# Performance work log

Measured on AMD Instinct MI355X. Metric: run time of the kernel, lower is better.

Reference implementation:

```python
import jax, jax.numpy as jnp
import numpy as np

D_HEAD = 64
IGNORE = -100000.0


def setup_inputs() -> dict:
    key = jax.random.key(0)
    ks = jax.random.split(key, 5)
    B, S, D, H, M = 2, 2048, 768, 12, D_HEAD
    scale = 0.05  # 'random_normal' keras init stddev
    return {
        "x": jax.random.normal(ks[0], (B, S, D), jnp.float32),
        "W_Q": jax.random.normal(ks[1], (H, D, M), jnp.float32) * scale,
        "b_Q": jnp.zeros((H, M), jnp.float32),
        "W_K": jax.random.normal(ks[2], (H, D, M), jnp.float32) * scale,
        "b_K": jnp.zeros((H, M), jnp.float32),
        "W_V": jax.random.normal(ks[3], (H, D, M), jnp.float32) * scale,
        "b_V": jnp.zeros((H, M), jnp.float32),
        "W_O": jax.random.normal(ks[4], (H, M, D), jnp.float32) * scale,
        "b_O": jnp.zeros((D,), jnp.float32),
    }


def reference(x, W_Q, b_Q, W_K, b_K, W_V, b_V, W_O, b_O):
    # q,k,v: [b, s, h, m]
    q = jnp.einsum("bqd,hdm->bqhm", x, W_Q) + b_Q
    k = jnp.einsum("bkd,hdm->bkhm", x, W_K) + b_K
    v = jnp.einsum("bkd,hdm->bkhm", x, W_V) + b_V
    # scores: [b, h, q, k], scaled by 1/sqrt(d_head)
    scores = jnp.einsum("bqhm,bkhm->bhqk", q, k) / jnp.sqrt(
        jnp.asarray(D_HEAD, q.dtype)
    )
    S = x.shape[1]
    # causal mask: strictly-upper-triangular positions set to IGNORE (-1e5),
    # matching tf.where(mask == 1, IGNORE, scores)
    causal = jnp.arange(S)[:, None] >= jnp.arange(S)[None, :]  # [q, k]
    scores = jnp.where(causal[None, None, :, :], scores, jnp.asarray(IGNORE, scores.dtype))
    pattern = jax.nn.softmax(scores, axis=-1)
    z = jnp.einsum("bhqk,bkhm->bqhm", pattern, v)
    attn_out = jnp.einsum("bqhm,hmd->bqd", z, W_O) + b_O
    return attn_out
```

## Files before the change

### kernel.cpp

```cpp
#include <hip/hip_runtime.h>
#include <hip/hip_bf16.h>
#include <cstdint>
#include <cstddef>

#define B_ 2
#define S_ 2048
#define D_ 768
#define H_ 12
#define M_ 64
#define BS_ (B_ * S_)
#define NQKV_ 2304
#define NCHUNK_ 80
#define TOTCHUNK_ (24 * NCHUNK_)

typedef __attribute__((ext_vector_type(8))) short bf16x8;
typedef __attribute__((ext_vector_type(4))) float f32x4;

__device__ __forceinline__ unsigned short f2bu(float f) {
    __hip_bfloat16 h = __float2bfloat16(f);
    unsigned short u;
    __builtin_memcpy(&u, &h, 2);
    return u;
}
__device__ __forceinline__ unsigned pack2(float a, float b) {
    return (unsigned)f2bu(a) | ((unsigned)f2bu(b) << 16);
}

__device__ __forceinline__ bf16x8 ld16(const unsigned short* p) {
    p = (const unsigned short*)__builtin_assume_aligned(p, 16);
    bf16x8 v; __builtin_memcpy(&v, p, 16); return v;
}
__device__ __forceinline__ uint4 ld16u(const unsigned short* p) {
    p = (const unsigned short*)__builtin_assume_aligned(p, 16);
    uint4 v; __builtin_memcpy(&v, p, 16); return v;
}
__device__ __forceinline__ void st16(unsigned short* p, uint4 v) {
    p = (unsigned short*)__builtin_assume_aligned(p, 16);
    __builtin_memcpy(p, &v, 16);
}
__device__ __forceinline__ void st8(unsigned short* p, uint2 v) {
    p = (unsigned short*)__builtin_assume_aligned(p, 8);
    __builtin_memcpy(p, &v, 8);
}
__device__ __forceinline__ float4 ldf4(const float* p) {
    p = (const float*)__builtin_assume_aligned(p, 16);
    float4 v; __builtin_memcpy(&v, p, 16); return v;
}
__device__ __forceinline__ void async16(const unsigned short* g, unsigned short* l) {
    __builtin_amdgcn_global_load_lds(
        (const __attribute__((address_space(1))) void*)g,
        (__attribute__((address_space(3))) void*)l, 16, 0, 0);
}
__device__ __forceinline__ void b82f(uint4 u, float* o) {
    o[0] = __uint_as_float(u.x << 16); o[1] = __uint_as_float(u.x & 0xffff0000u);
    o[2] = __uint_as_float(u.y << 16); o[3] = __uint_as_float(u.y & 0xffff0000u);
    o[4] = __uint_as_float(u.z << 16); o[5] = __uint_as_float(u.z & 0xffff0000u);
    o[6] = __uint_as_float(u.w << 16); o[7] = __uint_as_float(u.w & 0xffff0000u);
}

#define NEG_BIG (-3.0e38f)

__global__ void prep(const float* __restrict__ WQ, const float* __restrict__ WK,
                     const float* __restrict__ WV, const float* __restrict__ WO,
                     const float* __restrict__ x,
                     unsigned short* __restrict__ WT,
                     unsigned short* __restrict__ WOT,
                     unsigned short* __restrict__ xb)
{
    const int bx = blockIdx.x;
    if (bx < 216) {
        const int xx = bx % 9, yy = bx / 9;
        const int c  = xx * 256 + threadIdx.x;
        const int k0 = yy * 32;
        const int which = c / D_;
        const int r = c - which * D_;
        const int h = r >> 6, m = r & 63;
        const float* Wsel = (which == 0) ? WQ : (which == 1) ? WK : WV;
        const float* src = Wsel + (size_t)h * D_ * M_ + m;
        unsigned short* dst = WT + (size_t)c * D_ + k0;
        for (int i = 0; i < 32; i += 8) {
            float wv[8];
#pragma unroll
            for (int j = 0; j < 8; j++) wv[j] = src[(size_t)(k0 + i + j) * M_];
            uint4 pu;
            pu.x = pack2(wv[0], wv[1]); pu.y = pack2(wv[2], wv[3]);
            pu.z = pack2(wv[4], wv[5]); pu.w = pack2(wv[6], wv[7]);
            st16(dst + i, pu);
        }
    } else if (bx < 288) {
        const int b2 = bx - 216;
        const int xx = b2 % 3, yy = b2 / 3;
        const int c  = xx * 256 + threadIdx.x;
        const int k0 = yy * 32;
        unsigned short* dst = WOT + (size_t)c * D_ + k0;
        for (int i = 0; i < 32; i += 8) {
            float wv[8];
#pragma unroll
            for (int j = 0; j < 8; j++) wv[j] = WO[(size_t)(k0 + i + j) * D_ + c];
            uint4 pu;
            pu.x = pack2(wv[0], wv[1]); pu.y = pack2(wv[2], wv[3]);
            pu.z = pack2(wv[4], wv[5]); pu.w = pack2(wv[6], wv[7]);
            st16(dst + i, pu);
        }
    } else {
        const size_t i = ((size_t)(bx - 288) * 256 + threadIdx.x) * 16;
#pragma unroll
        for (int p = 0; p < 2; p++) {
            float4 a0 = ldf4(x + i + p * 8), a1 = ldf4(x + i + p * 8 + 4);
            uint4 u;
            u.x = pack2(a0.x, a0.y); u.y = pack2(a0.z, a0.w);
            u.z = pack2(a1.x, a1.y); u.w = pack2(a1.z, a1.w);
            st16(xb + i + p * 8, u);
        }
    }
}

__global__ __launch_bounds__(256, 2) void qkv_gemm(
    const unsigned short* __restrict__ xb,
    const unsigned short* __restrict__ WT,
    const float* __restrict__ bQ, const float* __restrict__ bK,
    const float* __restrict__ bV,
    unsigned short* __restrict__ qo, unsigned short* __restrict__ ko,
    unsigned short* __restrict__ vt)
{
    const int row0 = blockIdx.x * 128;
    const int col0 = blockIdx.y * 128;
    const int t = threadIdx.x;
    const int w = t >> 6, lane = t & 63, quad = lane >> 4, l16 = lane & 15;
    const int wrow0 = (w & 1) * 64, wcol0 = (w >> 1) * 64;

    __shared__ unsigned short Alds[128 * 64];
    __shared__ unsigned short Blds[128 * 64];

    f32x4 acc[4][4] = {};

    const unsigned short* asrc[4];
    const unsigned short* bsrc[4];
    int ldsoff[4];
#pragma unroll
    for (int q = 0; q < 4; q++) {
        const int cq = w * 256 + q * 64 + lane;
        const int row = cq >> 3, c = cq & 7;
        const int cs = c ^ (row & 7);
        asrc[q] = xb + (size_t)(row0 + row) * D_ + cs * 8;
        bsrc[q] = WT + (size_t)(col0 + row) * D_ + cs * 8;
        ldsoff[q] = (w * 256 + q * 64) * 8;
    }
    const int swz = (l16 & 7);

    for (int k0 = 0; k0 < D_; k0 += 64) {
#pragma unroll
        for (int q = 0; q < 4; q++) async16(asrc[q] + k0, Alds + ldsoff[q]);
#pragma unroll
        for (int q = 0; q < 4; q++) async16(bsrc[q] + k0, Blds + ldsoff[q]);
        __syncthreads();

        bf16x8 af[4][2], bfm[4][2];
#pragma unroll
        for (int rt = 0; rt < 4; rt++) {
            const int row = wrow0 + rt * 16 + l16;
#pragma unroll
            for (int hh = 0; hh < 2; hh++)
                af[rt][hh] = ld16(&Alds[row * 64 + ((hh * 4 + quad) ^ swz) * 8]);
        }
#pragma unroll
        for (int st = 0; st < 4; st++) {
            const int row = wcol0 + st * 16 + l16;
#pragma unroll
            for (int hh = 0; hh < 2; hh++)
                bfm[st][hh] = ld16(&Blds[row * 64 + ((hh * 4 + quad) ^ swz) * 8]);
        }
#pragma unroll
        for (int rt = 0; rt < 4; rt++)
#pragma unroll
            for (int st = 0; st < 4; st++) {
                acc[rt][st] = __builtin_amdgcn_mfma_f32_16x16x32_bf16(
                    af[rt][0], bfm[st][0], acc[rt][st], 0, 0, 0);
                acc[rt][st] = __builtin_amdgcn_mfma_f32_16x16x32_bf16(
                    af[rt][1], bfm[st][1], acc[rt][st], 0, 0, 0);
            }
        __syncthreads();
    }

    const int which = col0 / D_;
    const int colin = col0 - which * D_;

    if (which < 2) {
        const float* bias = (which == 0) ? bQ : bK;
        unsigned short* outp = (which == 0) ? qo : ko;
        const float scale = (which == 0) ? 0.125f : 1.0f;
#pragma unroll
        for (int st = 0; st < 4; st++) {
            const int cl = colin + wcol0 + st * 16 + l16;
            const int h = cl >> 6, m = cl & 63;
            const float bval = bias[cl];
#pragma unroll
            for (int rt = 0; rt < 4; rt++)
#pragma unroll
                for (int rr = 0; rr < 4; rr++) {
                    const int R = row0 + wrow0 + rt * 16 + quad * 4 + rr;
                    const int bb = R >> 11, s = R & (S_ - 1);
                    outp[(((size_t)bb * H_ + h) * S_ + s) * M_ + m] =
                        f2bu((acc[rt][st][rr] + bval) * scale);
                }
        }
    } else {
#pragma unroll
        for (int st = 0; st < 4; st++) {
            const int cl = colin + wcol0 + st * 16 + l16;
            const int h = cl >> 6, m = cl & 63;
            const float bval = bV[cl];
#pragma unroll
            for (int rt = 0; rt < 4; rt++) {
                const int R0 = row0 + wrow0 + rt * 16 + quad * 4;
                const int bb = R0 >> 11, s0 = R0 & (S_ - 1);
                uint2 v;
                v.x = pack2(acc[rt][st][0] + bval, acc[rt][st][1] + bval);
                v.y = pack2(acc[rt][st][2] + bval, acc[rt][st][3] + bval);
                st8(&vt[(((size_t)bb * H_ + h) * M_ + m) * S_ + s0], v);
            }
        }
    }
}

struct StageRegs { uint4 ka[4]; uint4 va[4]; };

__device__ __forceinline__ void load_tile(const unsigned short* kb,
                                          const unsigned short* vb,
                                          int t, StageRegs& s)
{
#pragma unroll
    for (int q = 0; q < 4; q++) {
        const int ci = q * 256 + t;
        s.ka[q] = ld16u(kb + (size_t)(ci >> 3) * M_ + (ci & 7) * 8);
    }
#pragma unroll
    for (int q = 0; q < 4; q++) {
        const int ci = q * 256 + t;
        s.va[q] = ld16u(vb + (size_t)(ci >> 4) * S_ + (ci & 15) * 8);
    }
}

__global__ __launch_bounds__(256, 3) void attn_split(
    const unsigned short* __restrict__ Q,
    const unsigned short* __restrict__ Kin,
    const unsigned short* __restrict__ Vt,
    unsigned short* __restrict__ Opart,
    float* __restrict__ ml)
{
    const int xx = blockIdx.x;
    const int bh = blockIdx.y;

    int qt, c, nc;
    if (xx < 8)       { qt = xx; c = 0; nc = 1; }
    else if (xx < 24) { int u = xx - 8;  qt = 8  + (u >> 1); c = u & 1;  nc = 2; }
    else if (xx < 48) { int u = xx - 24; qt = 16 + u / 3;    c = u % 3;  nc = 3; }
    else              { int u = xx - 48; qt = 24 + (u >> 2); c = u & 3;  nc = 4; }

    const int ci     = bh * NCHUNK_ + xx;
    const int kbeg   = c * 512;
    const int keyend = min((qt + 1) * 64, kbeg + 512);
    const int iters  = (keyend - kbeg + 127) >> 7;
    const bool lastchunk = (c == nc - 1);

    const int t = threadIdx.x;
    const int wave = t >> 6, lane = t & 63, quad = lane >> 4, l16 = lane & 15;

    const unsigned short* Qb  = Q   + ((size_t)bh * S_ + qt * 64) * M_;
    const unsigned short* Kb  = Kin + (size_t)bh * S_ * M_;
    const unsigned short* VtB = Vt  + (size_t)bh * M_ * S_;

    __shared__ unsigned short Klds[128][72];
    __shared__ unsigned short Vlds[64][136];
    __shared__ unsigned short Plds[4][16][136];

    bf16x8 qf[2];
    {
        const unsigned short* qrow = Qb + (size_t)(wave * 16 + l16) * M_;
        qf[0] = ld16(qrow + quad * 8);
        qf[1] = ld16(qrow + 32 + quad * 8);
    }

    f32x4 o_acc[4] = {};
    float mrow = NEG_BIG, lrow = 0.f;

    StageRegs sr;
    load_tile(Kb + (size_t)kbeg * M_, VtB + kbeg, t, sr);

    for (int it = 0; it < iters; it++) {
        __syncthreads();
#pragma unroll
        for (int q = 0; q < 4; q++) {
            const int cq = q * 256 + t;
            st16(&Klds[cq >> 3][(cq & 7) * 8], sr.ka[q]);
        }
#pragma unroll
        for (int q = 0; q < 4; q++) {
            const int cq = q * 256 + t;
            st16(&Vlds[cq >> 4][(cq & 15) * 8], sr.va[q]);
        }
        __syncthreads();

        if (it + 1 < iters) {
            const int key1 = kbeg + (it + 1) * 128;
            load_tile(Kb + (size_t)key1 * M_, VtB + key1, t, sr);
        }

        f32x4 s_acc[8];
#pragma unroll
        for (int st = 0; st < 8; st++) {
            f32x4 z4 = {0.f, 0.f, 0.f, 0.f};
            bf16x8 kb0 = ld16(&Klds[st * 16 + l16][quad * 8]);
            bf16x8 kb1 = ld16(&Klds[st * 16 + l16][32 + quad * 8]);
            z4 = __builtin_amdgcn_mfma_f32_16x16x32_bf16(kb0, qf[0], z4, 0, 0, 0);
            z4 = __builtin_amdgcn_mfma_f32_16x16x32_bf16(kb1, qf[1], z4, 0, 0, 0);
            s_acc[st] = z4;
        }

        if (lastchunk && it == iters - 1) {
            const int key0 = kbeg + it * 128 + quad * 4;
            const int qg = qt * 64 + wave * 16 + l16;
#pragma unroll
            for (int st = 0; st < 8; st++)
#pragma unroll
                for (int r = 0; r < 4; r++)
                    if (key0 + st * 16 + r > qg)
                        s_acc[st][r] = -1e30f;
        }

        float lmax = s_acc[0][0];
#pragma unroll
        for (int st = 0; st < 8; st++)
#pragma unroll
            for (int r = 0; r < 4; r++) lmax = fmaxf(lmax, s_acc[st][r]);
        lmax = fmaxf(lmax, __shfl_xor(lmax, 16, 64));
        lmax = fmaxf(lmax, __shfl_xor(lmax, 32, 64));

        const float mnew = fmaxf(mrow, lmax);
        const float alpha = __expf(mrow - mnew);
        mrow = mnew;

        float p[8][4];
        float psum = 0.f;
#pragma unroll
        for (int st = 0; st < 8; st++)
#pragma unroll
            for (int r = 0; r < 4; r++) {
                p[st][r] = __expf(s_acc[st][r] - mnew);
                psum += p[st][r];
            }
        psum += __shfl_xor(psum, 16, 64);
        psum += __shfl_xor(psum, 32, 64);
        lrow = lrow * alpha + psum;

#pragma unroll
        for (int stf = 0; stf < 4; stf++)
#pragma unroll
            for (int r = 0; r < 4; r++) o_acc[stf][r] *= alpha;

#pragma unroll
        for (int st = 0; st < 8; st++) {
            uint2 u;
            u.x = pack2(p[st][0], p[st][1]);
            u.y = pack2(p[st][2], p[st][3]);
            st8(&Plds[wave][l16][st * 16 + quad * 4], u);
        }

        __syncthreads();

        bf16x8 pt[4];
#pragma unroll
        for (int cc = 0; cc < 4; cc++)
            pt[cc] = ld16(&Plds[wave][l16][cc * 32 + quad * 8]);
#pragma unroll
        for (int stf = 0; stf < 4; stf++) {
#pragma unroll
            for (int cc = 0; cc < 4; cc++) {
                bf16x8 vb = ld16(&Vlds[stf * 16 + l16][cc * 32 + quad * 8]);
                o_acc[stf] = __builtin_amdgcn_mfma_f32_16x16x32_bf16(
                    vb, pt[cc], o_acc[stf], 0, 0, 0);
            }
        }
    }

    unsigned short* Op = Opart + (size_t)ci * 4096;
    const int q = wave * 16 + l16;
#pragma unroll
    for (int stf = 0; stf < 4; stf++) {
        uint2 u;
        u.x = pack2(o_acc[stf][0], o_acc[stf][1]);
        u.y = pack2(o_acc[stf][2], o_acc[stf][3]);
        st8(&Op[q * 64 + stf * 16 + quad * 4], u);
    }
    if (quad == 0) {
        ml[(size_t)ci * 128 + q]      = mrow;
        ml[(size_t)ci * 128 + 64 + q] = lrow;
    }
}

__global__ void combine(const unsigned short* __restrict__ Opart,
                        const float* __restrict__ ml,
                        unsigned short* __restrict__ Z)
{
    const int qt = blockIdx.x, bh = blockIdx.y;
    const int b = bh / H_, h = bh - b * H_;
    const int g = qt >> 3, r7 = qt & 7;
    const int nc = g + 1;
    const int base = bh * NCHUNK_ + qt + 4 * g * (g - 1) + r7 * g;

    const int t = threadIdx.x;
    const int q = t >> 2, fs = (t & 3) * 16;

    float m_c[4], l_c[4];
    float M = NEG_BIG;
    for (int c = 0; c < nc; c++) {
        m_c[c] = ml[(size_t)(base + c) * 128 + q];
        l_c[c] = ml[(size_t)(base + c) * 128 + 64 + q];
        M = fmaxf(M, m_c[c]);
    }
    float L = 0.f;
    float w_c[4];
    for (int c = 0; c < nc; c++) {
        w_c[c] = __expf(m_c[c] - M);
        L += l_c[c] * w_c[c];
    }
    const float invL = 1.0f / L;

    float o[16] = {};
    for (int c = 0; c < nc; c++) {
        const unsigned short* op =
            Opart + (size_t)(base + c) * 4096 + q * 64 + fs;
        const float wc = w_c[c];
        float f[8];
        b82f(ld16u(op), f);
#pragma unroll
        for (int j = 0; j < 8; j++) o[j] += wc * f[j];
        b82f(ld16u(op + 8), f);
#pragma unroll
        for (int j = 0; j < 8; j++) o[8 + j] += wc * f[j];
    }

    unsigned short* zp =
        Z + ((size_t)b * S_ + qt * 64 + q) * (H_ * M_) + h * M_ + fs;
    uint4 u0, u1;
    u0.x = pack2(o[0]*invL,  o[1]*invL);  u0.y = pack2(o[2]*invL,  o[3]*invL);
    u0.z = pack2(o[4]*invL,  o[5]*invL);  u0.w = pack2(o[6]*invL,  o[7]*invL);
    u1.x = pack2(o[8]*invL,  o[9]*invL);  u1.y = pack2(o[10]*invL, o[11]*invL);
    u1.z = pack2(o[12]*invL, o[13]*invL); u1.w = pack2(o[14]*invL, o[15]*invL);
    st16(zp, u0);
    st16(zp + 8, u1);
}

__global__ __launch_bounds__(256, 2) void oproj_gemm(
    const unsigned short* __restrict__ Zin,
    const unsigned short* __restrict__ WOT,
    const float* __restrict__ bO,
    float* __restrict__ out)
{
    const int row0 = blockIdx.x * 128;
    const int col0 = blockIdx.y * 128;
    const int t = threadIdx.x;
    const int w = t >> 6, lane = t & 63, quad = lane >> 4, l16 = lane & 15;
    const int wrow0 = (w & 1) * 64, wcol0 = (w >> 1) * 64;

    __shared__ unsigned short Alds[128 * 64];
    __shared__ unsigned short Blds[128 * 64];

    f32x4 acc[4][4] = {};

    const unsigned short* asrc[4];
    const unsigned short* bsrc[4];
    int ldsoff[4];
#pragma unroll
    for (int q = 0; q < 4; q++) {
        const int cq = w * 256 + q * 64 + lane;
        const int row = cq >> 3, c = cq & 7;
        const int cs = c ^ (row & 7);
        asrc[q] = Zin + (size_t)(row0 + row) * D_ + cs * 8;
        bsrc[q] = WOT + (size_t)(col0 + row) * D_ + cs * 8;
        ldsoff[q] = (w * 256 + q * 64) * 8;
    }
    const int swz = (l16 & 7);

    for (int k0 = 0; k0 < D_; k0 += 64) {
#pragma unroll
        for (int q = 0; q < 4; q++) async16(asrc[q] + k0, Alds + ldsoff[q]);
#pragma unroll
        for (int q = 0; q < 4; q++) async16(bsrc[q] + k0, Blds + ldsoff[q]);
        __syncthreads();

        bf16x8 af[4][2], bfm[4][2];
#pragma unroll
        for (int rt = 0; rt < 4; rt++) {
            const int row = wrow0 + rt * 16 + l16;
#pragma unroll
            for (int hh = 0; hh < 2; hh++)
                af[rt][hh] = ld16(&Alds[row * 64 + ((hh * 4 + quad) ^ swz) * 8]);
        }
#pragma unroll
        for (int st = 0; st < 4; st++) {
            const int row = wcol0 + st * 16 + l16;
#pragma unroll
            for (int hh = 0; hh < 2; hh++)
                bfm[st][hh] = ld16(&Blds[row * 64 + ((hh * 4 + quad) ^ swz) * 8]);
        }
#pragma unroll
        for (int rt = 0; rt < 4; rt++)
#pragma unroll
            for (int st = 0; st < 4; st++) {
                acc[rt][st] = __builtin_amdgcn_mfma_f32_16x16x32_bf16(
                    af[rt][0], bfm[st][0], acc[rt][st], 0, 0, 0);
                acc[rt][st] = __builtin_amdgcn_mfma_f32_16x16x32_bf16(
                    af[rt][1], bfm[st][1], acc[rt][st], 0, 0, 0);
            }
        __syncthreads();
    }

#pragma unroll
    for (int st = 0; st < 4; st++) {
        const int c = col0 + wcol0 + st * 16 + l16;
        const float bval = bO[c];
#pragma unroll
        for (int rt = 0; rt < 4; rt++)
#pragma unroll
            for (int rr = 0; rr < 4; rr++) {
                const int R = row0 + wrow0 + rt * 16 + quad * 4 + rr;
                out[(size_t)R * D_ + c] = acc[rt][st][rr] + bval;
            }
    }
}

extern "C" void kernel_launch(void* const* d_in, const int* in_sizes, int n_in,
                              void* d_out, int out_size, void* d_ws, size_t ws_size,
                              hipStream_t stream)
{
    const float* x  = (const float*)d_in[0];
    const float* WQ = (const float*)d_in[1];
    const float* bQ = (const float*)d_in[2];
    const float* WK = (const float*)d_in[3];
    const float* bK = (const float*)d_in[4];
    const float* WV = (const float*)d_in[5];
    const float* bV = (const float*)d_in[6];
    const float* WO = (const float*)d_in[7];
    const float* bO = (const float*)d_in[8];
    float* out = (float*)d_out;

    const size_t n = (size_t)B_ * H_ * S_ * M_;
    unsigned short* q_ws  = (unsigned short*)d_ws;
    unsigned short* k_ws  = q_ws + n;
    unsigned short* vt_ws = k_ws + n;
    unsigned short* z_ws  = vt_ws + n;
    unsigned short* WT    = z_ws + n;
    unsigned short* WOT   = WT + (size_t)NQKV_ * D_;
    unsigned short* xb    = WOT + (size_t)D_ * D_;
    unsigned short* Opart = xb + (size_t)BS_ * D_;
    float* mlbuf = (float*)(Opart + (size_t)TOTCHUNK_ * 4096);

    prep<<<dim3(1056), 256, 0, stream>>>(WQ, WK, WV, WO, x, WT, WOT, xb);
    qkv_gemm<<<dim3(BS_ / 128, NQKV_ / 128), 256, 0, stream>>>(
        xb, WT, bQ, bK, bV, q_ws, k_ws, vt_ws);
    attn_split<<<dim3(NCHUNK_, B_ * H_), 256, 0, stream>>>(
        q_ws, k_ws, vt_ws, Opart, mlbuf);
    combine<<<dim3(S_ / 64, B_ * H_), 256, 0, stream>>>(Opart, mlbuf, z_ws);
    oproj_gemm<<<dim3(BS_ / 128, D_ / 128), 256, 0, stream>>>(
        z_ws, WOT, bO, out);
}
```

Before: 166.1 us.

## Fuse split-KV combine into output projection and read V directly from global

Removes the separate combine kernel and the Z workspace. The output-projection GEMM now computes per-row chunk weights from the stored max/sum values and reduces the partial outputs into its A tile on the fly, head by head. In the attention kernel, V fragments are loaded straight from global memory instead of being staged in LDS, which frees shared memory and raises launch bounds to 4 blocks per CU. The softmax switches to exp2 with log2(e) folded into the Q scale. In exchange, the GEMM recomputes the combine for every column tile, and the uncached V loads depend on L2 hits.

```diff
diff --git a/kernel.cpp b/kernel.cpp
--- a/kernel.cpp
+++ b/kernel.cpp
@@ -12,6 +12,7 @@
 #define NQKV_ 2304
 #define NCHUNK_ 80
 #define TOTCHUNK_ (24 * NCHUNK_)
+#define QSCALE 0.18033688011f
 
 typedef __attribute__((ext_vector_type(8))) short bf16x8;
 typedef __attribute__((ext_vector_type(4))) float f32x4;
@@ -188,7 +189,7 @@
     if (which < 2) {
         const float* bias = (which == 0) ? bQ : bK;
         unsigned short* outp = (which == 0) ? qo : ko;
-        const float scale = (which == 0) ? 0.125f : 1.0f;
+        const float scale = (which == 0) ? QSCALE : 1.0f;
 #pragma unroll
         for (int st = 0; st < 4; st++) {
             const int cl = colin + wcol0 + st * 16 + l16;
@@ -223,25 +224,7 @@
     }
 }
 
-struct StageRegs { uint4 ka[4]; uint4 va[4]; };
-
-__device__ __forceinline__ void load_tile(const unsigned short* kb,
-                                          const unsigned short* vb,
-                                          int t, StageRegs& s)
-{
-#pragma unroll
-    for (int q = 0; q < 4; q++) {
-        const int ci = q * 256 + t;
-        s.ka[q] = ld16u(kb + (size_t)(ci >> 3) * M_ + (ci & 7) * 8);
-    }
-#pragma unroll
-    for (int q = 0; q < 4; q++) {
-        const int ci = q * 256 + t;
-        s.va[q] = ld16u(vb + (size_t)(ci >> 4) * S_ + (ci & 15) * 8);
-    }
-}
-
-__global__ __launch_bounds__(256, 3) void attn_split(
+__global__ __launch_bounds__(256, 4) void attn_split(
     const unsigned short* __restrict__ Q,
     const unsigned short* __restrict__ Kin,
     const unsigned short* __restrict__ Vt,
@@ -271,7 +254,6 @@
     const unsigned short* VtB = Vt  + (size_t)bh * M_ * S_;
 
     __shared__ unsigned short Klds[128][72];
-    __shared__ unsigned short Vlds[64][136];
     __shared__ unsigned short Plds[4][16][136];
 
     bf16x8 qf[2];
@@ -280,30 +262,37 @@
         qf[0] = ld16(qrow + quad * 8);
         qf[1] = ld16(qrow + 32 + quad * 8);
     }
+    const unsigned short* vrow[4];
+#pragma unroll
+    for (int stf = 0; stf < 4; stf++)
+        vrow[stf] = VtB + (size_t)(stf * 16 + l16) * S_ + quad * 8;
 
     f32x4 o_acc[4] = {};
     float mrow = NEG_BIG, lrow = 0.f;
 
-    StageRegs sr;
-    load_tile(Kb + (size_t)kbeg * M_, VtB + kbeg, t, sr);
+    uint4 ka[4];
+#pragma unroll
+    for (int q = 0; q < 4; q++) {
+        const int cq = q * 256 + t;
+        ka[q] = ld16u(Kb + (size_t)(kbeg + (cq >> 3)) * M_ + (cq & 7) * 8);
+    }
 
     for (int it = 0; it < iters; it++) {
-        __syncthreads();
+        const int key0 = kbeg + it * 128;
 #pragma unroll
         for (int q = 0; q < 4; q++) {
             const int cq = q * 256 + t;
-            st16(&Klds[cq >> 3][(cq & 7) * 8], sr.ka[q]);
-        }
-#pragma unroll
-        for (int q = 0; q < 4; q++) {
-            const int cq = q * 256 + t;
-            st16(&Vlds[cq >> 4][(cq & 15) * 8], sr.va[q]);
+            st16(&Klds[cq >> 3][(cq & 7) * 8], ka[q]);
         }
         __syncthreads();
 
         if (it + 1 < iters) {
-            const int key1 = kbeg + (it + 1) * 128;
-            load_tile(Kb + (size_t)key1 * M_, VtB + key1, t, sr);
+            const int key1 = key0 + 128;
+#pragma unroll
+            for (int q = 0; q < 4; q++) {
+                const int cq = q * 256 + t;
+                ka[q] = ld16u(Kb + (size_t)(key1 + (cq >> 3)) * M_ + (cq & 7) * 8);
+            }
         }
 
         f32x4 s_acc[8];
@@ -318,13 +307,13 @@
         }
 
         if (lastchunk && it == iters - 1) {
-            const int key0 = kbeg + it * 128 + quad * 4;
+            const int keyq = key0 + quad * 4;
             const int qg = qt * 64 + wave * 16 + l16;
 #pragma unroll
             for (int st = 0; st < 8; st++)
 #pragma unroll
                 for (int r = 0; r < 4; r++)
-                    if (key0 + st * 16 + r > qg)
+                    if (keyq + st * 16 + r > qg)
                         s_acc[st][r] = -1e30f;
         }
 
@@ -337,17 +326,16 @@
         lmax = fmaxf(lmax, __shfl_xor(lmax, 32, 64));
 
         const float mnew = fmaxf(mrow, lmax);
-        const float alpha = __expf(mrow - mnew);
+        const float alpha = exp2f(mrow - mnew);
         mrow = mnew;
 
-        float p[8][4];
         float psum = 0.f;
 #pragma unroll
         for (int st = 0; st < 8; st++)
 #pragma unroll
             for (int r = 0; r < 4; r++) {
-                p[st][r] = __expf(s_acc[st][r] - mnew);
-                psum += p[st][r];
+                s_acc[st][r] = exp2f(s_acc[st][r] - mnew);
+                psum += s_acc[st][r];
             }
         psum += __shfl_xor(psum, 16, 64);
         psum += __shfl_xor(psum, 32, 64);
@@ -361,8 +349,8 @@
 #pragma unroll
         for (int st = 0; st < 8; st++) {
             uint2 u;
-            u.x = pack2(p[st][0], p[st][1]);
-            u.y = pack2(p[st][2], p[st][3]);
+            u.x = pack2(s_acc[st][0], s_acc[st][1]);
+            u.y = pack2(s_acc[st][2], s_acc[st][3]);
             st8(&Plds[wave][l16][st * 16 + quad * 4], u);
         }
 
@@ -376,7 +364,7 @@
         for (int stf = 0; stf < 4; stf++) {
 #pragma unroll
             for (int cc = 0; cc < 4; cc++) {
-                bf16x8 vb = ld16(&Vlds[stf * 16 + l16][cc * 32 + quad * 8]);
+                bf16x8 vb = ld16(vrow[stf] + key0 + cc * 32);
                 o_acc[stf] = __builtin_amdgcn_mfma_f32_16x16x32_bf16(
                     vb, pt[cc], o_acc[stf], 0, 0, 0);
             }
@@ -398,61 +386,9 @@
     }
 }
 
-__global__ void combine(const unsigned short* __restrict__ Opart,
-                        const float* __restrict__ ml,
-                        unsigned short* __restrict__ Z)
-{
-    const int qt = blockIdx.x, bh = blockIdx.y;
-    const int b = bh / H_, h = bh - b * H_;
-    const int g = qt >> 3, r7 = qt & 7;
-    const int nc = g + 1;
-    const int base = bh * NCHUNK_ + qt + 4 * g * (g - 1) + r7 * g;
-
-    const int t = threadIdx.x;
-    const int q = t >> 2, fs = (t & 3) * 16;
-
-    float m_c[4], l_c[4];
-    float M = NEG_BIG;
-    for (int c = 0; c < nc; c++) {
-        m_c[c] = ml[(size_t)(base + c) * 128 + q];
-        l_c[c] = ml[(size_t)(base + c) * 128 + 64 + q];
-        M = fmaxf(M, m_c[c]);
-    }
-    float L = 0.f;
-    float w_c[4];
-    for (int c = 0; c < nc; c++) {
-        w_c[c] = __expf(m_c[c] - M);
-        L += l_c[c] * w_c[c];
-    }
-    const float invL = 1.0f / L;
-
-    float o[16] = {};
-    for (int c = 0; c < nc; c++) {
-        const unsigned short* op =
-            Opart + (size_t)(base + c) * 4096 + q * 64 + fs;
-        const float wc = w_c[c];
-        float f[8];
-        b82f(ld16u(op), f);
-#pragma unroll
-        for (int j = 0; j < 8; j++) o[j] += wc * f[j];
-        b82f(ld16u(op + 8), f);
-#pragma unroll
-        for (int j = 0; j < 8; j++) o[8 + j] += wc * f[j];
-    }
-
-    unsigned short* zp =
-        Z + ((size_t)b * S_ + qt * 64 + q) * (H_ * M_) + h * M_ + fs;
-    uint4 u0, u1;
-    u0.x = pack2(o[0]*invL,  o[1]*invL);  u0.y = pack2(o[2]*invL,  o[3]*invL);
-    u0.z = pack2(o[4]*invL,  o[5]*invL);  u0.w = pack2(o[6]*invL,  o[7]*invL);
-    u1.x = pack2(o[8]*invL,  o[9]*invL);  u1.y = pack2(o[10]*invL, o[11]*invL);
-    u1.z = pack2(o[12]*invL, o[13]*invL); u1.w = pack2(o[14]*invL, o[15]*invL);
-    st16(zp, u0);
-    st16(zp + 8, u1);
-}
-
 __global__ __launch_bounds__(256, 2) void oproj_gemm(
-    const unsigned short* __restrict__ Zin,
+    const unsigned short* __restrict__ Opart,
+    const float* __restrict__ ml,
     const unsigned short* __restrict__ WOT,
     const float* __restrict__ bO,
     float* __restrict__ out)
@@ -463,30 +399,72 @@
     const int w = t >> 6, lane = t & 63, quad = lane >> 4, l16 = lane & 15;
     const int wrow0 = (w & 1) * 64, wcol0 = (w >> 1) * 64;
 
-    __shared__ unsigned short Alds[128 * 64];
+    __shared__ unsigned short Alds[128][72];
     __shared__ unsigned short Blds[128 * 64];
+    __shared__ float wn[12][128][4];
 
     f32x4 acc[4][4] = {};
 
-    const unsigned short* asrc[4];
     const unsigned short* bsrc[4];
-    int ldsoff[4];
+    int ldsoffB[4];
 #pragma unroll
     for (int q = 0; q < 4; q++) {
         const int cq = w * 256 + q * 64 + lane;
         const int row = cq >> 3, c = cq & 7;
         const int cs = c ^ (row & 7);
-        asrc[q] = Zin + (size_t)(row0 + row) * D_ + cs * 8;
         bsrc[q] = WOT + (size_t)(col0 + row) * D_ + cs * 8;
-        ldsoff[q] = (w * 256 + q * 64) * 8;
+        ldsoffB[q] = (w * 256 + q * 64) * 8;
     }
     const int swz = (l16 & 7);
 
-    for (int k0 = 0; k0 < D_; k0 += 64) {
-#pragma unroll
-        for (int q = 0; q < 4; q++) async16(asrc[q] + k0, Alds + ldsoff[q]);
-#pragma unroll
-        for (int q = 0; q < 4; q++) async16(bsrc[q] + k0, Blds + ldsoff[q]);
+    for (int id = t; id < 12 * 128; id += 256) {
+        const int h = id >> 7, row = id & 127;
+        const int R = row0 + row, bb = R >> 11, s = R & (S_ - 1);
+        const int qt = s >> 6, g = qt >> 3, r7 = qt & 7, nc = g + 1;
+        const int base = (bb * H_ + h) * NCHUNK_ + qt + 4 * g * (g - 1) + r7 * g;
+        const int q = s & 63;
+        float m_c[4], l_c[4], M = NEG_BIG;
+        for (int c = 0; c < nc; c++) {
+            m_c[c] = ml[(size_t)(base + c) * 128 + q];
+            l_c[c] = ml[(size_t)(base + c) * 128 + 64 + q];
+            M = fmaxf(M, m_c[c]);
+        }
+        float L = 0.f, wgt[4];
+        for (int c = 0; c < nc; c++) {
+            wgt[c] = exp2f(m_c[c] - M);
+            L += l_c[c] * wgt[c];
+        }
+        const float invL = 1.0f / L;
+        for (int c = 0; c < nc; c++) wn[h][row][c] = wgt[c] * invL;
+    }
+    __syncthreads();
+
+    for (int h = 0; h < 12; h++) {
+#pragma unroll
+        for (int q = 0; q < 4; q++)
+            async16(bsrc[q] + h * 64, Blds + ldsoffB[q]);
+
+#pragma unroll
+        for (int qq = 0; qq < 4; qq++) {
+            const int cq = w * 256 + qq * 64 + lane;
+            const int row = cq >> 3, ms = (cq & 7) * 8;
+            const int R = row0 + row, bb = R >> 11, s = R & (S_ - 1);
+            const int qt = s >> 6, g = qt >> 3, r7 = qt & 7, nc = g + 1;
+            const int base = (bb * H_ + h) * NCHUNK_ + qt + 4 * g * (g - 1) + r7 * g;
+            const int q = s & 63;
+            float o8[8] = {};
+            for (int c = 0; c < nc; c++) {
+                float f[8];
+                b82f(ld16u(Opart + (size_t)(base + c) * 4096 + q * 64 + ms), f);
+                const float wc = wn[h][row][c];
+#pragma unroll
+                for (int j = 0; j < 8; j++) o8[j] += wc * f[j];
+            }
+            uint4 u;
+            u.x = pack2(o8[0], o8[1]); u.y = pack2(o8[2], o8[3]);
+            u.z = pack2(o8[4], o8[5]); u.w = pack2(o8[6], o8[7]);
+            st16(&Alds[row][ms], u);
+        }
         __syncthreads();
 
         bf16x8 af[4][2], bfm[4][2];
@@ -495,7 +473,7 @@
             const int row = wrow0 + rt * 16 + l16;
 #pragma unroll
             for (int hh = 0; hh < 2; hh++)
-                af[rt][hh] = ld16(&Alds[row * 64 + ((hh * 4 + quad) ^ swz) * 8]);
+                af[rt][hh] = ld16(&Alds[row][hh * 32 + quad * 8]);
         }
 #pragma unroll
         for (int st = 0; st < 4; st++) {
@@ -549,8 +527,7 @@
     unsigned short* q_ws  = (unsigned short*)d_ws;
     unsigned short* k_ws  = q_ws + n;
     unsigned short* vt_ws = k_ws + n;
-    unsigned short* z_ws  = vt_ws + n;
-    unsigned short* WT    = z_ws + n;
+    unsigned short* WT    = vt_ws + n;
     unsigned short* WOT   = WT + (size_t)NQKV_ * D_;
     unsigned short* xb    = WOT + (size_t)D_ * D_;
     unsigned short* Opart = xb + (size_t)BS_ * D_;
@@ -561,7 +538,6 @@
         xb, WT, bQ, bK, bV, q_ws, k_ws, vt_ws);
     attn_split<<<dim3(NCHUNK_, B_ * H_), 256, 0, stream>>>(
         q_ws, k_ws, vt_ws, Opart, mlbuf);
-    combine<<<dim3(S_ / 64, B_ * H_), 256, 0, stream>>>(Opart, mlbuf, z_ws);
     oproj_gemm<<<dim3(BS_ / 128, D_ / 128), 256, 0, stream>>>(
-        z_ws, WOT, bO, out);
-}
+        Opart, mlbuf, WOT, bO, out);
+}
```

Result: slower. 246.9 us (+48.6%).
